# Kernel optimization log

Hardware: AMD Instinct MI355X
Metric: run time of the kernel (lower is better)

Reference implementation:

```python
import jax, jax.numpy as jnp
import numpy as np

EPS = 1e-5  # BatchNorm eps (torch default)

def _bn(x, gamma, beta):
    # training-mode BatchNorm over the edge/node (leading) axis, biased var
    mean = x.mean(axis=0, keepdims=True)
    var = x.var(axis=0, keepdims=True)
    return (x - mean) * jax.lax.rsqrt(var + EPS) * gamma + beta

def _silu(x):
    return x * jax.nn.sigmoid(x)

def setup_inputs() -> dict:
    N, E, H, NH = 50000, 800000, 128, 4
    HD = H // NH
    key = jax.random.key(0)
    ks = jax.random.split(key, 8)
    x = jax.random.normal(ks[0], (N, H), dtype=jnp.float32)
    weight = jax.random.uniform(ks[1], (N, 1), dtype=jnp.float32)  # positive fraction weights
    src = jax.random.randint(ks[2], (E,), 0, N)
    dst = jax.random.randint(ks[3], (E,), 0, N)
    # f: Linear(2H, 1) + BN(1)
    Wf = jax.random.normal(ks[4], (2 * H, 1), dtype=jnp.float32) * 0.05
    bf = jnp.zeros((1,), jnp.float32)
    f_gamma = jnp.ones((1,), jnp.float32)
    f_beta = jnp.zeros((1,), jnp.float32)
    # g: NH heads of Linear(2H, HD) + BN(HD), stacked on leading head axis
    Wg = jax.random.normal(ks[5], (NH, 2 * H, HD), dtype=jnp.float32) * 0.05
    bg = jnp.zeros((NH, HD), jnp.float32)
    g_gamma = jnp.ones((NH, HD), jnp.float32)
    g_beta = jnp.zeros((NH, HD), jnp.float32)
    # bn_nodes: BN(H)
    n_gamma = jnp.ones((H,), jnp.float32)
    n_beta = jnp.zeros((H,), jnp.float32)
    return dict(x=x, weight=weight, src=src, dst=dst, Wf=Wf, bf=bf,
                f_gamma=f_gamma, f_beta=f_beta, Wg=Wg, bg=bg,
                g_gamma=g_gamma, g_beta=g_beta, n_gamma=n_gamma, n_beta=n_beta)

def reference(x, weight, src, dst, Wf, bf, f_gamma, f_beta, Wg, bg, g_gamma, g_beta, n_gamma, n_beta):
    N = x.shape[0]
    E = src.shape[0]
    # per-edge concat of src/dst node features: [E, 2H]
    hihj = jnp.concatenate([x[src], x[dst]], axis=-1)
    # attention logit f(hihj) = SiLU(BN(Linear)) then exp: [E, 1]
    exp_e = jnp.exp(_silu(_bn(hihj @ Wf + bf, f_gamma, f_beta)))
    # weighted softmax-like normalization over incoming edges of each dst node
    we = weight[src] * exp_e                                   # [E, 1]
    sum_w_exp = jax.ops.segment_sum(we, dst, num_segments=N)   # [N, 1]
    a = we / sum_w_exp[dst]                                    # [E, 1]
    # multi-head message: a_ij * SiLU(BN(Linear_h(hihj))) per head, concat
    z = jnp.einsum('ed,hdk->ehk', hihj, Wg) + bg               # [E, NH, HD]
    z = _silu(_bn(z, g_gamma, g_beta))
    msg = (a[:, :, None] * z).reshape(E, -1)                   # [E, H]
    h = jax.ops.segment_sum(msg, dst, num_segments=N)          # [N, H]
    out = _bn(h, n_gamma, n_beta) + x                          # residual
    return out
```

## Files before the change

kernel.cpp:

```cpp
#include <hip/hip_runtime.h>
#include <hip/hip_bf16.h>
#include <math.h>

#define HDIM 128
#define PAD 64
typedef unsigned short ushort_t;
typedef unsigned int uint_t;
typedef __attribute__((ext_vector_type(8))) short bf16x8;
typedef __attribute__((ext_vector_type(4))) float f32x4;
typedef __attribute__((ext_vector_type(2))) float v2f;

__device__ __forceinline__ float wave_allreduce(float v){
  #pragma unroll
  for (int o = 1; o < 64; o <<= 1) v += __shfl_xor(v, o);
  return v;
}

__device__ __forceinline__ ushort_t f2bf(float f){
  uint_t u = __float_as_uint(f);
  uint_t r = (u + 0x7fffu + ((u >> 16) & 1u)) >> 16;
  return (ushort_t)r;
}

__device__ __forceinline__ v2f bf2(uint_t u){
  v2f r;
  r.x = __uint_as_float(u << 16);
  r.y = __uint_as_float(u & 0xffff0000u);
  return r;
}

__global__ __launch_bounds__(128) void k_wpack(const float* __restrict__ Wg,
    const float* __restrict__ Wf, ushort_t* __restrict__ W2t,
    int* __restrict__ cnt, int N){
  int b = blockIdx.x;
  int k = threadIdx.x;
  if (b < 272){
    float val;
    if (b < 128)       val = Wg[(size_t)(b >> 5) * 8192 + k * 32 + (b & 31)];
    else if (b < 256){ int c2 = b - 128;
                       val = Wg[(size_t)(c2 >> 5) * 8192 + (k + 128) * 32 + (c2 & 31)]; }
    else if (b == 256) val = Wf[k];
    else if (b == 257) val = Wf[128 + k];
    else               val = 0.f;
    W2t[(size_t)b * 128 + k] = f2bf(val);
  } else {
    int i = (b - 272) * 128 + k;
    if (i < N) cnt[i] = 0;
  }
}

__global__ __launch_bounds__(256) void k_gemm(const float* __restrict__ x,
    const ushort_t* __restrict__ W2t, const float* __restrict__ weight,
    ushort_t* __restrict__ Pb, ushort_t* __restrict__ Qb,
    float* __restrict__ v, float2* __restrict__ uw2, int N){
  int wid = __builtin_amdgcn_readfirstlane(threadIdx.x >> 6);
  int lane = threadIdx.x & 63;
  int quad = lane >> 4, col = lane & 15;
  int n_base = (blockIdx.x * 4 + wid) * 16;
  if (n_base >= N) return;
  f32x4 acc[17];
  #pragma unroll
  for (int t = 0; t < 17; ++t) acc[t] = (f32x4){0.f, 0.f, 0.f, 0.f};
  int row = n_base + col;
  int rowc = row < N ? row : N - 1;
  const float* xr = x + (size_t)rowc * HDIM + quad * 8;
  #pragma unroll
  for (int kk = 0; kk < 4; ++kk){
    float4 a0 = *(const float4*)(xr + kk * 32);
    float4 a1 = *(const float4*)(xr + kk * 32 + 4);
    bf16x8 af;
    af[0] = (short)f2bf(a0.x); af[1] = (short)f2bf(a0.y);
    af[2] = (short)f2bf(a0.z); af[3] = (short)f2bf(a0.w);
    af[4] = (short)f2bf(a1.x); af[5] = (short)f2bf(a1.y);
    af[6] = (short)f2bf(a1.z); af[7] = (short)f2bf(a1.w);
    const ushort_t* wb = W2t + (size_t)col * 128 + kk * 32 + quad * 8;
    #pragma unroll
    for (int ct = 0; ct < 17; ++ct){
      bf16x8 bfr = *(const bf16x8*)(wb + (size_t)ct * 16 * 128);
      acc[ct] = __builtin_amdgcn_mfma_f32_16x16x32_bf16(af, bfr, acc[ct], 0, 0, 0);
    }
  }
  #pragma unroll
  for (int ct = 0; ct < 16; ++ct){
    int c = ct * 16 + col;
    #pragma unroll
    for (int r = 0; r < 4; ++r){
      int n = n_base + quad * 4 + r;
      if (n < N){
        ushort_t valb = f2bf(acc[ct][r]);
        if (c < 128) Pb[(size_t)n * HDIM + c] = valb;
        else         Qb[(size_t)n * HDIM + (c - 128)] = valb;
      }
    }
  }
  #pragma unroll
  for (int r = 0; r < 4; ++r){
    int n = n_base + quad * 4 + r;
    if (n < N){
      float val = acc[16][r];
      if (col == 0)      uw2[n] = make_float2(val, weight[n]);
      else if (col == 1) v[n] = val;
    }
  }
}

__global__ __launch_bounds__(256) void k_fillx(const int* __restrict__ src,
    const int* __restrict__ dst, int* __restrict__ cnt, int* __restrict__ es,
    int E, int N){
  int part = blockIdx.x & 7;
  int nch = gridDim.x >> 3;
  int chunk = blockIdx.x >> 3;
  int Npp = (N + 7) >> 3;
  int lo = part * Npp;
  int hi = lo + Npp; if (hi > N) hi = N;
  int stride = nch * 256;
  for (int e = chunk * 256 + threadIdx.x; e < E; e += stride){
    int d = dst[e];
    if (d >= lo && d < hi){
      int c = atomicAdd(&cnt[d], 1);
      if (c < PAD) es[(size_t)d * PAD + c] = src[e];
    }
  }
}

__global__ __launch_bounds__(256) void k_gstats(const ushort_t* __restrict__ Pb,
    const ushort_t* __restrict__ Qb, const float* __restrict__ v,
    const float2* __restrict__ uw2, const int* __restrict__ es,
    const int* __restrict__ cnt, float* __restrict__ pstatG, int N, int NW){
  int lane = threadIdx.x & 63;
  int wid = __builtin_amdgcn_readfirstlane(threadIdx.x >> 6);
  int wg = blockIdx.x * 4 + wid;
  const uint_t* Pu = (const uint_t*)Pb;
  const uint_t* Qu = (const uint_t*)Qb;
  v2f gs = {0.f, 0.f}, gq = {0.f, 0.f};
  float fs = 0.f, fq = 0.f;
  for (int n = wg; n < N; n += NW){
    int dn = cnt[n]; dn = dn < PAD ? dn : PAD;
    v2f q = bf2(Qu[(size_t)n * 64 + lane]);
    float vn = v[n];
    int sj = 0;
    if (lane < dn){
      sj = es[(size_t)n * PAD + lane];
      float t = uw2[sj].x + vn;
      fs += t; fq = fmaf(t, t, fq);
    }
    int j = 0;
    for (; j + 3 < dn; j += 4){
      int s0 = __shfl(sj, j),     s1 = __shfl(sj, j + 1);
      int s2 = __shfl(sj, j + 2), s3 = __shfl(sj, j + 3);
      uint_t p0 = Pu[(size_t)s0 * 64 + lane];
      uint_t p1 = Pu[(size_t)s1 * 64 + lane];
      uint_t p2 = Pu[(size_t)s2 * 64 + lane];
      uint_t p3 = Pu[(size_t)s3 * 64 + lane];
      v2f y0 = bf2(p0) + q, y1 = bf2(p1) + q, y2 = bf2(p2) + q, y3 = bf2(p3) + q;
      gs += y0 + y1 + y2 + y3;
      gq += y0 * y0; gq += y1 * y1; gq += y2 * y2; gq += y3 * y3;
    }
    for (; j < dn; ++j){
      int s0 = __shfl(sj, j);
      v2f y0 = bf2(Pu[(size_t)s0 * 64 + lane]) + q;
      gs += y0; gq += y0 * y0;
    }
  }
  fs = wave_allreduce(fs); fq = wave_allreduce(fq);
  float* pb = pstatG + (size_t)wg * 258;
  *(float2*)&pb[2 * lane]       = make_float2(gs.x, gs.y);
  *(float2*)&pb[128 + 2 * lane] = make_float2(gq.x, gq.y);
  if (lane == 0){ pb[256] = fs; pb[257] = fq; }
}

__global__ __launch_bounds__(256) void k_redfin1(const float* __restrict__ pstatG,
    int NW, const float* __restrict__ g_gamma, const float* __restrict__ g_beta,
    const float* __restrict__ f_gamma, const float* __restrict__ f_beta,
    float* __restrict__ fin, long long E){
  int j = blockIdx.x;
  int c1 = (j < 128) ? j : 256;
  int c2 = (j < 128) ? 128 + j : 257;
  double s1 = 0, s2 = 0;
  for (int b = threadIdx.x; b < NW; b += 256){
    const float* pb = pstatG + (size_t)b * 258;
    s1 += (double)pb[c1]; s2 += (double)pb[c2];
  }
  __shared__ double m1[256], m2[256];
  m1[threadIdx.x] = s1; m2[threadIdx.x] = s2;
  __syncthreads();
  for (int o = 128; o; o >>= 1){
    if (threadIdx.x < o){ m1[threadIdx.x] += m1[threadIdx.x + o];
                          m2[threadIdx.x] += m2[threadIdx.x + o]; }
    __syncthreads();
  }
  if (threadIdx.x == 0){
    double m = m1[0] / (double)E;
    double var = m2[0] / (double)E - m * m;
    if (j < 128){
      float sc = (float)((double)g_gamma[j] / sqrt(var + 1e-5));
      fin[2 + j] = sc; fin[130 + j] = g_beta[j] - (float)m * sc;
    } else {
      float sc = (float)((double)f_gamma[0] / sqrt(var + 1e-5));
      fin[0] = sc; fin[1] = f_beta[0] - (float)m * sc;
    }
  }
}

__global__ __launch_bounds__(256) void k_msg(const ushort_t* __restrict__ Pb,
    const ushort_t* __restrict__ Qb, const float* __restrict__ v,
    const float2* __restrict__ uw2, const int* __restrict__ es,
    const int* __restrict__ cnt, const float* __restrict__ fin,
    float* __restrict__ h, float* __restrict__ pstatH, int N, int NW){
  int lane = threadIdx.x & 63;
  int wid = __builtin_amdgcn_readfirstlane(threadIdx.x >> 6);
  int wg = blockIdx.x * 4 + wid;
  const uint_t* Pu = (const uint_t*)Pb;
  const uint_t* Qu = (const uint_t*)Qb;
  float fsc = fin[0], fsh = fin[1];
  v2f gsc = {fin[2 + 2 * lane], fin[3 + 2 * lane]};
  v2f gsh = {fin[130 + 2 * lane], fin[131 + 2 * lane]};
  v2f hs = {0.f, 0.f}, hq = {0.f, 0.f};
  for (int n = wg; n < N; n += NW){
    int dn = cnt[n]; dn = dn < PAD ? dn : PAD;
    float vn = v[n];
    int sj = 0; float wj = 0.f;
    if (lane < dn){
      sj = es[(size_t)n * PAD + lane];
      float2 uw = uw2[sj];
      float t = fmaf(uw.x + vn, fsc, fsh);
      float sl = t * __builtin_amdgcn_rcpf(1.f + __expf(-t));
      wj = uw.y * __expf(sl);
    }
    float sw = wave_allreduce(wj);
    wj *= (dn > 0) ? (1.f / sw) : 0.f;
    v2f q = bf2(Qu[(size_t)n * 64 + lane]);
    v2f acc = {0.f, 0.f};
    int j = 0;
    for (; j + 3 < dn; j += 4){
      int s0 = __shfl(sj, j),     s1 = __shfl(sj, j + 1);
      int s2 = __shfl(sj, j + 2), s3 = __shfl(sj, j + 3);
      float a0 = __shfl(wj, j),     a1 = __shfl(wj, j + 1);
      float a2 = __shfl(wj, j + 2), a3 = __shfl(wj, j + 3);
      uint_t p0 = Pu[(size_t)s0 * 64 + lane];
      uint_t p1 = Pu[(size_t)s1 * 64 + lane];
      uint_t p2 = Pu[(size_t)s2 * 64 + lane];
      uint_t p3 = Pu[(size_t)s3 * 64 + lane];
      {
        v2f y = (bf2(p0) + q) * gsc + gsh;
        float e0 = __expf(-y.x), e1 = __expf(-y.y);
        float d0 = 1.f + e0, d1 = 1.f + e1;
        float r = __builtin_amdgcn_rcpf(d0 * d1) * a0;
        v2f z; z.x = y.x * d1; z.y = y.y * d0;
        acc += z * (v2f){r, r};
      }
      {
        v2f y = (bf2(p1) + q) * gsc + gsh;
        float e0 = __expf(-y.x), e1 = __expf(-y.y);
        float d0 = 1.f + e0, d1 = 1.f + e1;
        float r = __builtin_amdgcn_rcpf(d0 * d1) * a1;
        v2f z; z.x = y.x * d1; z.y = y.y * d0;
        acc += z * (v2f){r, r};
      }
      {
        v2f y = (bf2(p2) + q) * gsc + gsh;
        float e0 = __expf(-y.x), e1 = __expf(-y.y);
        float d0 = 1.f + e0, d1 = 1.f + e1;
        float r = __builtin_amdgcn_rcpf(d0 * d1) * a2;
        v2f z; z.x = y.x * d1; z.y = y.y * d0;
        acc += z * (v2f){r, r};
      }
      {
        v2f y = (bf2(p3) + q) * gsc + gsh;
        float e0 = __expf(-y.x), e1 = __expf(-y.y);
        float d0 = 1.f + e0, d1 = 1.f + e1;
        float r = __builtin_amdgcn_rcpf(d0 * d1) * a3;
        v2f z; z.x = y.x * d1; z.y = y.y * d0;
        acc += z * (v2f){r, r};
      }
    }
    for (; j < dn; ++j){
      int s0 = __shfl(sj, j);
      float a0 = __shfl(wj, j);
      v2f y = (bf2(Pu[(size_t)s0 * 64 + lane]) + q) * gsc + gsh;
      float e0 = __expf(-y.x), e1 = __expf(-y.y);
      float d0 = 1.f + e0, d1 = 1.f + e1;
      float r = __builtin_amdgcn_rcpf(d0 * d1) * a0;
      v2f z; z.x = y.x * d1; z.y = y.y * d0;
      acc += z * (v2f){r, r};
    }
    *(float2*)&h[(size_t)n * 128 + 2 * lane] = make_float2(acc.x, acc.y);
    hs += acc; hq += acc * acc;
  }
  float* pb = pstatH + (size_t)wg * 256;
  *(float2*)&pb[2 * lane]       = make_float2(hs.x, hs.y);
  *(float2*)&pb[128 + 2 * lane] = make_float2(hq.x, hq.y);
}

__global__ __launch_bounds__(256) void k_redfin2(const float* __restrict__ pstatH,
    int NW, const float* __restrict__ n_gamma, const float* __restrict__ n_beta,
    float* __restrict__ fin, int N){
  int j = blockIdx.x;
  double s1 = 0, s2 = 0;
  for (int b = threadIdx.x; b < NW; b += 256){
    const float* pb = pstatH + (size_t)b * 256;
    s1 += (double)pb[j]; s2 += (double)pb[128 + j];
  }
  __shared__ double m1[256], m2[256];
  m1[threadIdx.x] = s1; m2[threadIdx.x] = s2;
  __syncthreads();
  for (int o = 128; o; o >>= 1){
    if (threadIdx.x < o){ m1[threadIdx.x] += m1[threadIdx.x + o];
                          m2[threadIdx.x] += m2[threadIdx.x + o]; }
    __syncthreads();
  }
  if (threadIdx.x == 0){
    double m = m1[0] / (double)N;
    double var = m2[0] / (double)N - m * m;
    float sc = (float)((double)n_gamma[j] / sqrt(var + 1e-5));
    fin[258 + j] = sc; fin[386 + j] = n_beta[j] - (float)m * sc;
  }
}

__global__ __launch_bounds__(256) void k_out(const float* __restrict__ h,
    const float* __restrict__ x, const float* __restrict__ fin,
    float* __restrict__ out, int total4){
  int i = blockIdx.x * 256 + threadIdx.x;
  if (i >= total4) return;
  const float4* h4 = (const float4*)h; const float4* x4 = (const float4*)x;
  float4 hv = h4[i], xv = x4[i];
  int c = (i * 4) & 127;
  float4 o;
  o.x = fmaf(hv.x, fin[258 + c],     fin[386 + c])     + xv.x;
  o.y = fmaf(hv.y, fin[258 + c + 1], fin[386 + c + 1]) + xv.y;
  o.z = fmaf(hv.z, fin[258 + c + 2], fin[386 + c + 2]) + xv.z;
  o.w = fmaf(hv.w, fin[258 + c + 3], fin[386 + c + 3]) + xv.w;
  ((float4*)out)[i] = o;
}

extern "C" void kernel_launch(void* const* d_in, const int* in_sizes, int n_in,
                              void* d_out, int out_size, void* d_ws, size_t ws_size,
                              hipStream_t stream){
  const float* x       = (const float*)d_in[0];
  const float* weight  = (const float*)d_in[1];
  const int*   src     = (const int*)d_in[2];
  const int*   dst     = (const int*)d_in[3];
  const float* Wf      = (const float*)d_in[4];
  const float* f_gamma = (const float*)d_in[6];
  const float* f_beta  = (const float*)d_in[7];
  const float* Wg      = (const float*)d_in[8];
  const float* g_gamma = (const float*)d_in[10];
  const float* g_beta  = (const float*)d_in[11];
  const float* n_gamma = (const float*)d_in[12];
  const float* n_beta  = (const float*)d_in[13];
  float* out = (float*)d_out;

  int N = in_sizes[0] / HDIM;
  int E = in_sizes[2];

  char* ws = (char*)d_ws;
  size_t off = 0;
  auto alloc = [&](size_t bytes)->char*{
    char* p = ws + off; off = (off + bytes + 255) & ~(size_t)255; return p;
  };
  ushort_t* Pb    = (ushort_t*)alloc((size_t)N * HDIM * 2);
  ushort_t* Qb    = (ushort_t*)alloc((size_t)N * HDIM * 2);
  float* h        = (float*)alloc((size_t)N * HDIM * 4);
  float* v        = (float*)alloc((size_t)N * 4);
  float2* uw2     = (float2*)alloc((size_t)N * 8);
  int* es         = (int*)alloc((size_t)N * PAD * 4);
  ushort_t* W2t   = (ushort_t*)alloc((size_t)272 * 128 * 2);
  int* cnt        = (int*)alloc((size_t)N * 4);
  const int NWB = 2048;
  const int NW  = NWB * 4;
  float*  pstatG = (float*)alloc((size_t)NW * 258 * 4);
  float*  pstatH = (float*)alloc((size_t)NW * 256 * 4);
  float*  fin    = (float*)alloc(514 * 4);

  k_wpack  <<<272 + (N + 127) / 128, 128, 0, stream>>>(Wg, Wf, W2t, cnt, N);
  k_gemm   <<<(N + 63) / 64, 256, 0, stream>>>(x, W2t, weight, Pb, Qb, v, uw2, N);
  k_fillx  <<<8 * 1024, 256, 0, stream>>>(src, dst, cnt, es, E, N);
  k_gstats <<<NWB, 256, 0, stream>>>(Pb, Qb, v, uw2, es, cnt, pstatG, N, NW);
  k_redfin1<<<129, 256, 0, stream>>>(pstatG, NW, g_gamma, g_beta, f_gamma, f_beta, fin, (long long)E);
  k_msg    <<<NWB, 256, 0, stream>>>(Pb, Qb, v, uw2, es, cnt, fin, h, pstatH, N, NW);
  k_redfin2<<<128, 256, 0, stream>>>(pstatH, NW, n_gamma, n_beta, fin, N);
  k_out    <<<(N * HDIM / 4 + 255) / 256, 256, 0, stream>>>(h, x, fin, out, N * HDIM / 4);
}
```

Measured before the change: 317.9 us.

## Merge node GEMM and edge bucketing into one kernel, split GEMM tiles across waves

The projection GEMM and the dst-bucketing fill, which do not depend on each other, now run as one launch. The first GB blocks compute the GEMM and the rest do the atomic fill, so the two can run concurrently and one launch gap goes away. Within the GEMM, each 16-row strip is now split across two waves (8 and 9 column tiles) instead of one wave holding all 17 accumulators. This lowers register pressure and raises wave count, at the cost of each wave reloading and converting the x rows. The fill grid shrinks from 8192 to 4096 blocks, which gives more edges per thread.

```diff
diff --git a/kernel.cpp b/kernel.cpp
--- a/kernel.cpp
+++ b/kernel.cpp
@@ -49,76 +49,87 @@
   }
 }
 
-__global__ __launch_bounds__(256) void k_gemm(const float* __restrict__ x,
+__global__ __launch_bounds__(256) void k_gemmfill(const float* __restrict__ x,
     const ushort_t* __restrict__ W2t, const float* __restrict__ weight,
     ushort_t* __restrict__ Pb, ushort_t* __restrict__ Qb,
-    float* __restrict__ v, float2* __restrict__ uw2, int N){
-  int wid = __builtin_amdgcn_readfirstlane(threadIdx.x >> 6);
-  int lane = threadIdx.x & 63;
-  int quad = lane >> 4, col = lane & 15;
-  int n_base = (blockIdx.x * 4 + wid) * 16;
-  if (n_base >= N) return;
-  f32x4 acc[17];
-  #pragma unroll
-  for (int t = 0; t < 17; ++t) acc[t] = (f32x4){0.f, 0.f, 0.f, 0.f};
-  int row = n_base + col;
-  int rowc = row < N ? row : N - 1;
-  const float* xr = x + (size_t)rowc * HDIM + quad * 8;
-  #pragma unroll
-  for (int kk = 0; kk < 4; ++kk){
-    float4 a0 = *(const float4*)(xr + kk * 32);
-    float4 a1 = *(const float4*)(xr + kk * 32 + 4);
-    bf16x8 af;
-    af[0] = (short)f2bf(a0.x); af[1] = (short)f2bf(a0.y);
-    af[2] = (short)f2bf(a0.z); af[3] = (short)f2bf(a0.w);
-    af[4] = (short)f2bf(a1.x); af[5] = (short)f2bf(a1.y);
-    af[6] = (short)f2bf(a1.z); af[7] = (short)f2bf(a1.w);
-    const ushort_t* wb = W2t + (size_t)col * 128 + kk * 32 + quad * 8;
+    float* __restrict__ v, float2* __restrict__ uw2,
+    const int* __restrict__ src, const int* __restrict__ dst,
+    int* __restrict__ cnt, int* __restrict__ es,
+    int N, int E, int GB){
+  if ((int)blockIdx.x < GB){
+    int wid = __builtin_amdgcn_readfirstlane(threadIdx.x >> 6);
+    int lane = threadIdx.x & 63;
+    int quad = lane >> 4, col = lane & 15;
+    int strip = blockIdx.x * 2 + (wid >> 1);
+    int half = wid & 1;
+    int n_base = strip * 16;
+    if (n_base >= N) return;
+    int tbeg = half * 8;
+    int ntile = half ? 9 : 8;
+    f32x4 acc[9];
     #pragma unroll
-    for (int ct = 0; ct < 17; ++ct){
-      bf16x8 bfr = *(const bf16x8*)(wb + (size_t)ct * 16 * 128);
-      acc[ct] = __builtin_amdgcn_mfma_f32_16x16x32_bf16(af, bfr, acc[ct], 0, 0, 0);
-    }
-  }
-  #pragma unroll
-  for (int ct = 0; ct < 16; ++ct){
-    int c = ct * 16 + col;
+    for (int t = 0; t < 9; ++t) acc[t] = (f32x4){0.f, 0.f, 0.f, 0.f};
+    int row = n_base + col;
+    int rowc = row < N ? row : N - 1;
+    const float* xr = x + (size_t)rowc * HDIM + quad * 8;
     #pragma unroll
-    for (int r = 0; r < 4; ++r){
-      int n = n_base + quad * 4 + r;
-      if (n < N){
-        ushort_t valb = f2bf(acc[ct][r]);
-        if (c < 128) Pb[(size_t)n * HDIM + c] = valb;
-        else         Qb[(size_t)n * HDIM + (c - 128)] = valb;
-      }
-    }
-  }
-  #pragma unroll
-  for (int r = 0; r < 4; ++r){
-    int n = n_base + quad * 4 + r;
-    if (n < N){
-      float val = acc[16][r];
-      if (col == 0)      uw2[n] = make_float2(val, weight[n]);
-      else if (col == 1) v[n] = val;
-    }
-  }
-}
-
-__global__ __launch_bounds__(256) void k_fillx(const int* __restrict__ src,
-    const int* __restrict__ dst, int* __restrict__ cnt, int* __restrict__ es,
-    int E, int N){
-  int part = blockIdx.x & 7;
-  int nch = gridDim.x >> 3;
-  int chunk = blockIdx.x >> 3;
-  int Npp = (N + 7) >> 3;
-  int lo = part * Npp;
-  int hi = lo + Npp; if (hi > N) hi = N;
-  int stride = nch * 256;
-  for (int e = chunk * 256 + threadIdx.x; e < E; e += stride){
-    int d = dst[e];
-    if (d >= lo && d < hi){
-      int c = atomicAdd(&cnt[d], 1);
-      if (c < PAD) es[(size_t)d * PAD + c] = src[e];
+    for (int kk = 0; kk < 4; ++kk){
+      float4 a0 = *(const float4*)(xr + kk * 32);
+      float4 a1 = *(const float4*)(xr + kk * 32 + 4);
+      bf16x8 af;
+      af[0] = (short)f2bf(a0.x); af[1] = (short)f2bf(a0.y);
+      af[2] = (short)f2bf(a0.z); af[3] = (short)f2bf(a0.w);
+      af[4] = (short)f2bf(a1.x); af[5] = (short)f2bf(a1.y);
+      af[6] = (short)f2bf(a1.z); af[7] = (short)f2bf(a1.w);
+      const ushort_t* wb = W2t + (size_t)(tbeg * 16) * 128 + (size_t)col * 128 + kk * 32 + quad * 8;
+      #pragma unroll
+      for (int t = 0; t < 9; ++t){
+        if (t < ntile){
+          bf16x8 bfr = *(const bf16x8*)(wb + (size_t)t * 16 * 128);
+          acc[t] = __builtin_amdgcn_mfma_f32_16x16x32_bf16(af, bfr, acc[t], 0, 0, 0);
+        }
+      }
+    }
+    #pragma unroll
+    for (int t = 0; t < 8; ++t){
+      int ct = tbeg + t;
+      int c = ct * 16 + col;
+      #pragma unroll
+      for (int r = 0; r < 4; ++r){
+        int n = n_base + quad * 4 + r;
+        if (n < N){
+          ushort_t valb = f2bf(acc[t][r]);
+          if (c < 128) Pb[(size_t)n * HDIM + c] = valb;
+          else         Qb[(size_t)n * HDIM + (c - 128)] = valb;
+        }
+      }
+    }
+    if (half){
+      #pragma unroll
+      for (int r = 0; r < 4; ++r){
+        int n = n_base + quad * 4 + r;
+        if (n < N){
+          float val = acc[8][r];
+          if (col == 0)      uw2[n] = make_float2(val, weight[n]);
+          else if (col == 1) v[n] = val;
+        }
+      }
+    }
+  } else {
+    int bi = blockIdx.x - GB;
+    int part = bi & 7;
+    int nch = (gridDim.x - GB) >> 3;
+    int chunk = bi >> 3;
+    int Npp = (N + 7) >> 3;
+    int lo = part * Npp;
+    int hi = lo + Npp; if (hi > N) hi = N;
+    int stride = nch * 256;
+    for (int e = chunk * 256 + threadIdx.x; e < E; e += stride){
+      int d = dst[e];
+      if (d >= lo && d < hi){
+        int c = atomicAdd(&cnt[d], 1);
+        if (c < PAD) es[(size_t)d * PAD + c] = src[e];
+      }
     }
   }
 }
@@ -372,12 +383,15 @@
   float*  pstatH = (float*)alloc((size_t)NW * 256 * 4);
   float*  fin    = (float*)alloc(514 * 4);
 
-  k_wpack  <<<272 + (N + 127) / 128, 128, 0, stream>>>(Wg, Wf, W2t, cnt, N);
-  k_gemm   <<<(N + 63) / 64, 256, 0, stream>>>(x, W2t, weight, Pb, Qb, v, uw2, N);
-  k_fillx  <<<8 * 1024, 256, 0, stream>>>(src, dst, cnt, es, E, N);
-  k_gstats <<<NWB, 256, 0, stream>>>(Pb, Qb, v, uw2, es, cnt, pstatG, N, NW);
-  k_redfin1<<<129, 256, 0, stream>>>(pstatG, NW, g_gamma, g_beta, f_gamma, f_beta, fin, (long long)E);
-  k_msg    <<<NWB, 256, 0, stream>>>(Pb, Qb, v, uw2, es, cnt, fin, h, pstatH, N, NW);
-  k_redfin2<<<128, 256, 0, stream>>>(pstatH, NW, n_gamma, n_beta, fin, N);
-  k_out    <<<(N * HDIM / 4 + 255) / 256, 256, 0, stream>>>(h, x, fin, out, N * HDIM / 4);
-}
+  int GB = (N + 31) / 32;
+  const int FB = 4096;
+
+  k_wpack   <<<272 + (N + 127) / 128, 128, 0, stream>>>(Wg, Wf, W2t, cnt, N);
+  k_gemmfill<<<GB + FB, 256, 0, stream>>>(x, W2t, weight, Pb, Qb, v, uw2,
+                                          src, dst, cnt, es, N, E, GB);
+  k_gstats  <<<NWB, 256, 0, stream>>>(Pb, Qb, v, uw2, es, cnt, pstatG, N, NW);
+  k_redfin1 <<<129, 256, 0, stream>>>(pstatG, NW, g_gamma, g_beta, f_gamma, f_beta, fin, (long long)E);
+  k_msg     <<<NWB, 256, 0, stream>>>(Pb, Qb, v, uw2, es, cnt, fin, h, pstatH, N, NW);
+  k_redfin2 <<<128, 256, 0, stream>>>(pstatH, NW, n_gamma, n_beta, fin, N);
+  k_out     <<<(N * HDIM / 4 + 255) / 256, 256, 0, stream>>>(h, x, fin, out, N * HDIM / 4);
+}
```

Result: faster. 302.2 us (-4.9%).
